# Kernel tuning notes

Hardware: AMD Instinct MI355X
Metric: run time of the kernel (lower is better)

## Reference

```python
import jax, jax.numpy as jnp
import numpy as np

FP8_MAX = 448.0  # float8_e4m3fn max
BLOCK = 128


def _quant_blocks_1d(x, bs=BLOCK, eps=1e-12):
    """Block-wise (along last dim) fp8 e4m3 quantization of activations.
    x: (M, K) float32 -> (x_q_f32 (M,K) on fp8 grid, scales (M, K//bs))."""
    M, K = x.shape
    xb = x.reshape(M, K // bs, bs)
    amax = jnp.max(jnp.abs(xb), axis=-1)                     # (M, Kb)
    s = jnp.maximum(amax / FP8_MAX, eps)                     # (M, Kb)
    xq = jnp.clip(xb / s[..., None], -FP8_MAX, FP8_MAX)
    xq = xq.astype(jnp.float8_e4m3fn).astype(jnp.float32)    # round to fp8 grid
    return xq.reshape(M, K), s


def _quant_weight_2d(w, bs=BLOCK, eps=1e-12):
    """2D block-wise fp8 quantization of weight (out, in) -> fp8-grid values + (Nb,Kb) scales."""
    N, K = w.shape
    wb = w.reshape(N // bs, bs, K // bs, bs)
    amax = jnp.max(jnp.abs(wb), axis=(1, 3))                 # (Nb, Kb)
    s = jnp.maximum(amax / FP8_MAX, eps)
    wq = jnp.clip(wb / s[:, None, :, None], -FP8_MAX, FP8_MAX)
    wq = wq.astype(jnp.float8_e4m3fn).astype(jnp.float32)
    return wq.reshape(N, K), s


def setup_inputs() -> dict:
    key = jax.random.key(0)
    kx, kw = jax.random.split(key)
    M, K, N = 4096, 2048, 8192
    x = jax.random.normal(kx, (M, K), dtype=jnp.float32)
    w = jax.random.normal(kw, (N, K), dtype=jnp.float32) * 0.02
    w_q, w_s = _quant_weight_2d(w)  # pre-quantized at "construction" time
    return {"x": x, "w_q": w_q, "w_s": w_s}


def reference(x, w_q, w_s):
    """FP8Linear forward (Triton path math): quantize x block-wise to fp8,
    block-scaled fp8 GEMM against fp8 weight with (Nb,Kb) weight scales.
    Math is identical to dequant-then-GEMM with fp32 accumulation."""
    bs = BLOCK
    M, K = x.shape
    N = w_q.shape[0]
    x_q, x_s = _quant_blocks_1d(x, bs)                        # (M,K), (M,K//bs)
    # dequantize (fold scales back in) — same values the fused kernel computes
    x_deq = (x_q.reshape(M, K // bs, bs) * x_s[..., None]).reshape(M, K)
    w_deq = (w_q.reshape(N // bs, bs, K // bs, bs) * w_s[:, None, :, None]).reshape(N, K)
    out = x_deq @ w_deq.T                                     # (M, N), fp32 accum
    return out
```

## Files before the change

### kernel.cpp

```cpp
#include <hip/hip_runtime.h>
#include <cstdint>
#include <cstddef>

static constexpr int M = 4096, K = 2048, N = 8192;
static constexpr int KBLK = K / 128;

#define GLOBAL_AS __attribute__((address_space(1)))
#define LDS_AS    __attribute__((address_space(3)))

typedef float f32x4 __attribute__((ext_vector_type(4)));
typedef int   i32x4 __attribute__((ext_vector_type(4)));
typedef int   i32x8 __attribute__((ext_vector_type(8)));


__device__ inline float fp8_e4m3_rne(float a) {
    float mag = fminf(fabsf(a), 448.0f);
    float r;
    if (mag < 0.015625f) {
        r = rintf(mag * 512.0f) * (1.0f / 512.0f);
    } else {
        uint32_t u = __float_as_uint(mag);
        u = (u + ((u >> 20) & 1u) + 0x7FFFFu) & 0xFFF00000u;
        r = fminf(__uint_as_float(u), 448.0f);
    }
    return copysignf(r, a);
}


__global__ void quant_x_kernel(const float* __restrict__ x, uint8_t* __restrict__ xq,
                               float* __restrict__ sxT) {
    int task = blockIdx.x * 8 + (threadIdx.x >> 5);
    int sub  = threadIdx.x & 31;
    int row = task >> 4;
    int kb  = task & 15;
    const float* p = x + (size_t)row * K + kb * 128 + sub * 4;
    float4 v = *reinterpret_cast<const float4*>(p);
    float amax = fmaxf(fmaxf(fabsf(v.x), fabsf(v.y)), fmaxf(fabsf(v.z), fabsf(v.w)));
    #pragma unroll
    for (int off = 16; off; off >>= 1) amax = fmaxf(amax, __shfl_xor(amax, off));
    float s = fmaxf(amax / 448.0f, 1e-12f);
    float q0 = fminf(fmaxf(v.x / s, -448.f), 448.f);
    float q1 = fminf(fmaxf(v.y / s, -448.f), 448.f);
    float q2 = fminf(fmaxf(v.z / s, -448.f), 448.f);
    float q3 = fminf(fmaxf(v.w / s, -448.f), 448.f);
    uint32_t pk = __builtin_amdgcn_cvt_pk_fp8_f32(q0, q1, 0, false);
    pk = __builtin_amdgcn_cvt_pk_fp8_f32(q2, q3, pk, true);
    *reinterpret_cast<uint32_t*>(xq + (size_t)row * K + kb * 128 + sub * 4) = pk;
    if (sub == 0) sxT[(size_t)kb * M + row] = s;
}

__global__ void quant_w_kernel(const float* __restrict__ wq, uint8_t* __restrict__ w8) {
    size_t i = ((size_t)blockIdx.x * blockDim.x + threadIdx.x) * 8;
    float4 a = *reinterpret_cast<const float4*>(wq + i);
    float4 b = *reinterpret_cast<const float4*>(wq + i + 4);
    uint32_t lo = __builtin_amdgcn_cvt_pk_fp8_f32(a.x, a.y, 0, false);
    lo = __builtin_amdgcn_cvt_pk_fp8_f32(a.z, a.w, lo, true);
    uint32_t hi = __builtin_amdgcn_cvt_pk_fp8_f32(b.x, b.y, 0, false);
    hi = __builtin_amdgcn_cvt_pk_fp8_f32(b.z, b.w, hi, true);
    uint2 o; o.x = lo; o.y = hi;
    *reinterpret_cast<uint2*>(w8 + i) = o;
}


__device__ __forceinline__ void stageA8(const uint8_t* __restrict__ g,
                                        uint8_t* l, int h, int tid) {
    #pragma unroll
    for (int i = 0; i < 2; ++i) {
        int t2 = tid + i * 512;
        int lr = t2 >> 3;
        int qs = t2 & 7;
        int r  = (lr >> 6) * 128 + h * 64 + (lr & 63);
        int s  = qs ^ (r & 7);
        int ks = ((s & 3) << 1) | (s >> 2);
        __builtin_amdgcn_global_load_lds(
            (const GLOBAL_AS uint32_t*)(g + (size_t)r * K + (ks << 4)),
            (LDS_AS uint32_t*)(l + r * 128 + qs * 16), 16, 0, 0);
    }
}

__device__ __forceinline__ void stageB8(const uint8_t* __restrict__ g,
                                        uint8_t* l, int h, int tid) {
    #pragma unroll
    for (int i = 0; i < 2; ++i) {
        int t2 = tid + i * 512;
        int lr = t2 >> 3;
        int qs = t2 & 7;
        int r  = (lr >> 5) * 64 + h * 32 + (lr & 31);
        int s  = qs ^ (r & 7);
        int ks = ((s & 3) << 1) | (s >> 2);
        __builtin_amdgcn_global_load_lds(
            (const GLOBAL_AS uint32_t*)(g + (size_t)r * K + (ks << 4)),
            (LDS_AS uint32_t*)(l + r * 128 + qs * 16), 16, 0, 0);
    }
}

#define LOAD_A(MH)                                                                \
  _Pragma("unroll")                                                               \
  for (int m = 0; m < 4; ++m) {                                                   \
    int row = wr * 128 + (MH) * 64 + m * 16 + (lane & 15);                        \
    const char* rp = (const char*)lAp + row * 128;                                \
    i32x4 lo = *(const i32x4*)(rp + (((lg)     ^ (row & 7)) << 4));               \
    i32x4 hi = *(const i32x4*)(rp + (((4 | lg) ^ (row & 7)) << 4));               \
    af[m] = __builtin_shufflevector(lo, hi, 0, 1, 2, 3, 4, 5, 6, 7);              \
    xs[m] = sxl[t * 256 + wr * 128 + (MH) * 64 + m * 16 + (lane & 15)];           \
  }

#define LOAD_B(NH)                                                                \
  _Pragma("unroll")                                                               \
  for (int n = 0; n < 2; ++n) {                                                   \
    int row = wc * 64 + (NH) * 32 + n * 16 + (lane & 15);                         \
    const char* rp = (const char*)lBp + row * 128;                                \
    i32x4 lo = *(const i32x4*)(rp + (((lg)     ^ (row & 7)) << 4));               \
    i32x4 hi = *(const i32x4*)(rp + (((4 | lg) ^ (row & 7)) << 4));               \
    bfr[n] = __builtin_shufflevector(lo, hi, 0, 1, 2, 3, 4, 5, 6, 7);             \
  }

#define QCOMP(MH, NH)                                                             \
  {                                                                               \
    f32x4 P[4][2];                                                                \
    __builtin_amdgcn_s_setprio(1);                                                \
    _Pragma("unroll")                                                             \
    for (int m = 0; m < 4; ++m)                                                   \
      _Pragma("unroll")                                                           \
      for (int n = 0; n < 2; ++n)                                                 \
        P[m][n] = __builtin_amdgcn_mfma_scale_f32_16x16x128_f8f6f4(               \
            bfr[n], af[m], zf4, 0, 0, 0, 0x7F7F7F7F, 0, 0x7F7F7F7F);              \
    __builtin_amdgcn_s_setprio(0);                                                \
    _Pragma("unroll")                                                             \
    for (int m = 0; m < 4; ++m) {                                                 \
      float sm = xs[m] * wst;                                                     \
      _Pragma("unroll")                                                           \
      for (int n = 0; n < 2; ++n)                                                 \
        acc[(MH) * 4 + m][(NH) * 2 + n] += sm * P[m][n];                          \
    }                                                                             \
  }

__global__ __launch_bounds__(512, 2) void gemm_kernel(
    const uint8_t* __restrict__ A, const uint8_t* __restrict__ B,
    const float* __restrict__ sxT_g, const float* __restrict__ Ws,
    float* __restrict__ C) {
    __shared__ uint8_t lA[2][256 * 128];
    __shared__ uint8_t lB[2][256 * 128];
    __shared__ float   sxl[KBLK * 256];
    __shared__ float   wsl[32];

    int cpx = gridDim.x >> 3;
    int sw  = (blockIdx.x & 7) * cpx + (blockIdx.x >> 3);
    int tm = sw & 15;
    int tn = sw >> 4;
    int row0 = tm * 256, col0 = tn * 256;

    int tid = threadIdx.x;
    int wid = tid >> 6, lane = tid & 63;
    int lg  = lane >> 4;
    int wr = wid >> 2, wc = wid & 3;

    const uint8_t* Ag = A + (size_t)row0 * K;
    const uint8_t* Bg = B + (size_t)col0 * K;

    f32x4 acc[8][4] = {};
    const f32x4 zf4 = {0.f, 0.f, 0.f, 0.f};

    if (tid < 32)
        __builtin_amdgcn_global_load_lds(
            (const GLOBAL_AS uint32_t*)(Ws + (tn * 2 + (tid >> 4)) * KBLK + (tid & 15)),
            (LDS_AS uint32_t*)(wsl + tid), 4, 0, 0);
    #pragma unroll
    for (int i = 0; i < 2; ++i) {
        int idx = tid + i * 512;
        __builtin_amdgcn_global_load_lds(
            (const GLOBAL_AS uint32_t*)(sxT_g + (size_t)(idx >> 6) * M + row0 + (idx & 63) * 4),
            (LDS_AS uint32_t*)(sxl + idx * 4), 16, 0, 0);
    }
    stageA8(Ag, lA[0], 0, tid);
    stageA8(Ag, lA[0], 1, tid);
    stageB8(Bg, lB[0], 0, tid);
    stageB8(Bg, lB[0], 1, tid);
    __syncthreads();

    for (int t = 0; t < KBLK; ++t) {
        const uint8_t* lAp = lA[t & 1];
        const uint8_t* lBp = lB[t & 1];
        uint8_t* sA = lA[(t + 1) & 1];
        uint8_t* sB = lB[(t + 1) & 1];
        int tn1 = (t + 1 < KBLK) ? (t + 1) : 0;
        const uint8_t* gA = Ag + (size_t)tn1 * 128;
        const uint8_t* gB = Bg + (size_t)tn1 * 128;
        bool stg = (t + 1 < KBLK);
        i32x8 af[4], bfr[2];
        float xs[4];
        float wst = wsl[(wc >> 1) * KBLK + t];

        LOAD_A(0); LOAD_B(0);
        if (stg) { stageA8(gA, sA, 0, tid); stageB8(gB, sB, 0, tid); }
        QCOMP(0, 0);
        LOAD_B(1);
        if (stg) stageB8(gB, sB, 1, tid);
        QCOMP(0, 1);
        LOAD_A(1);
        if (stg) stageA8(gA, sA, 1, tid);
        QCOMP(1, 1);
        LOAD_B(0);
        QCOMP(1, 0);

        __syncthreads();
    }

    #pragma unroll
    for (int m = 0; m < 8; ++m)
        #pragma unroll
        for (int j = 0; j < 4; ++j) {
            int rr = row0 + wr * 128 + m * 16 + (lane & 15);
            int cc = col0 + wc * 64 + j * 16 + (lane >> 4) * 4;
            *reinterpret_cast<f32x4*>(&C[(size_t)rr * N + cc]) = acc[m][j];
        }
}


__global__ void xs_kernel(const float* __restrict__ x, float* __restrict__ xs) {
    int task = blockIdx.x * 4 + (threadIdx.x >> 6);
    int lane = threadIdx.x & 63;
    int row = task >> 4, kb = task & 15;
    float2 v = *reinterpret_cast<const float2*>(x + (size_t)row * K + kb * 128 + lane * 2);
    float amax = fmaxf(fabsf(v.x), fabsf(v.y));
    #pragma unroll
    for (int off = 32; off; off >>= 1) amax = fmaxf(amax, __shfl_xor(amax, off));
    if (lane == 0) xs[row * KBLK + kb] = fmaxf(amax / 448.0f, 1e-12f);
}

__global__ __launch_bounds__(256) void fallback_gemm(const float* __restrict__ x,
                                                     const float* __restrict__ wq,
                                                     const float* __restrict__ wsc,
                                                     const float* __restrict__ xs,
                                                     float* __restrict__ C) {
    __shared__ float As[64][128];
    __shared__ float Bs[64][128];
    int tm = blockIdx.x % (M / 64), tn = blockIdx.x / (M / 64);
    int row0 = tm * 64, col0 = tn * 64;
    int tid = threadIdx.x;
    int tr = tid >> 4, tc = tid & 15;
    float acc[4][4] = {};
    for (int kb = 0; kb < KBLK; ++kb) {
        int k0 = kb * 128;
        __syncthreads();
        for (int t = tid * 4; t < 64 * 128; t += 256 * 4) {
            int r = t >> 7, c = t & 127;
            float4 va = *reinterpret_cast<const float4*>(x + (size_t)(row0 + r) * K + k0 + c);
            float sa = xs[(row0 + r) * KBLK + kb];
            va.x = fp8_e4m3_rne(va.x / sa) * sa; va.y = fp8_e4m3_rne(va.y / sa) * sa;
            va.z = fp8_e4m3_rne(va.z / sa) * sa; va.w = fp8_e4m3_rne(va.w / sa) * sa;
            *reinterpret_cast<float4*>(&As[r][c]) = va;
            float4 vb = *reinterpret_cast<const float4*>(wq + (size_t)(col0 + r) * K + k0 + c);
            float sb = wsc[((col0 + r) >> 7) * KBLK + kb];
            vb.x *= sb; vb.y *= sb; vb.z *= sb; vb.w *= sb;
            *reinterpret_cast<float4*>(&Bs[r][c]) = vb;
        }
        __syncthreads();
        for (int kk = 0; kk < 128; ++kk) {
            float a[4], b[4];
            #pragma unroll
            for (int i = 0; i < 4; ++i) a[i] = As[tr * 4 + i][kk];
            #pragma unroll
            for (int j = 0; j < 4; ++j) b[j] = Bs[tc * 4 + j][kk];
            #pragma unroll
            for (int i = 0; i < 4; ++i)
                #pragma unroll
                for (int j = 0; j < 4; ++j) acc[i][j] += a[i] * b[j];
        }
    }
    #pragma unroll
    for (int i = 0; i < 4; ++i)
        #pragma unroll
        for (int j = 0; j < 4; ++j)
            C[(size_t)(row0 + tr * 4 + i) * N + col0 + tc * 4 + j] = acc[i][j];
}


extern "C" void kernel_launch(void* const* d_in, const int* in_sizes, int n_in,
                              void* d_out, int out_size, void* d_ws, size_t ws_size,
                              hipStream_t stream) {
    const float* x  = (const float*)d_in[0];
    const float* wq = (const float*)d_in[1];
    const float* ws = (const float*)d_in[2];
    float* out = (float*)d_out;

    size_t need_fast = (size_t)M * K + (size_t)N * K + (size_t)KBLK * M * 4;
    if (ws_size >= need_fast) {
        uint8_t* xq8 = (uint8_t*)d_ws;
        uint8_t* w8  = xq8 + (size_t)M * K;
        float*   sxT = (float*)(w8 + (size_t)N * K);
        quant_x_kernel<<<M * KBLK / 8, 256, 0, stream>>>(x, xq8, sxT);
        quant_w_kernel<<<(int)(((size_t)N * K / 8) / 256), 256, 0, stream>>>(wq, w8);
        gemm_kernel<<<(M / 256) * (N / 256), 512, 0, stream>>>(xq8, w8, sxT, ws, out);
    } else if (ws_size >= (size_t)M * KBLK * 4) {
        float* xs = (float*)d_ws;
        xs_kernel<<<M * KBLK / 4, 256, 0, stream>>>(x, xs);
        fallback_gemm<<<(M / 64) * (N / 64), 256, 0, stream>>>(x, wq, ws, xs, out);
    }
}
```

Measured before the change: 115.4 us.

## Software-pipeline MFMA batches with rescale and fragment loads in GEMM loop

Restructures the per-K-block inner loop so that each batch of scaled MFMAs is issued before the previous batch's per-block rescale FMAs and the next fragment LDS loads. This lets VALU rescale work and LDS reads overlap with matrix-core execution. All four global-to-LDS staging calls for the next tile are now issued together up front, and the s_setprio hints are removed. In exchange the kernel holds more live registers (double B fragments, two scale arrays, two partial-product sets), which raises register pressure under the 512x2 launch bound.

```diff
diff --git a/kernel.cpp b/kernel.cpp
--- a/kernel.cpp
+++ b/kernel.cpp
@@ -94,45 +94,42 @@
     }
 }
 
-#define LOAD_A(MH)                                                                \
+#define LOAD_AF(MH, AFV, XSV)                                                     \
   _Pragma("unroll")                                                               \
   for (int m = 0; m < 4; ++m) {                                                   \
     int row = wr * 128 + (MH) * 64 + m * 16 + (lane & 15);                        \
     const char* rp = (const char*)lAp + row * 128;                                \
     i32x4 lo = *(const i32x4*)(rp + (((lg)     ^ (row & 7)) << 4));               \
     i32x4 hi = *(const i32x4*)(rp + (((4 | lg) ^ (row & 7)) << 4));               \
-    af[m] = __builtin_shufflevector(lo, hi, 0, 1, 2, 3, 4, 5, 6, 7);              \
-    xs[m] = sxl[t * 256 + wr * 128 + (MH) * 64 + m * 16 + (lane & 15)];           \
+    AFV[m] = __builtin_shufflevector(lo, hi, 0, 1, 2, 3, 4, 5, 6, 7);             \
+    XSV[m] = sxl[t * 256 + wr * 128 + (MH) * 64 + m * 16 + (lane & 15)];          \
   }
 
-#define LOAD_B(NH)                                                                \
+#define LOAD_BF(NH, BFV)                                                          \
   _Pragma("unroll")                                                               \
   for (int n = 0; n < 2; ++n) {                                                   \
     int row = wc * 64 + (NH) * 32 + n * 16 + (lane & 15);                         \
     const char* rp = (const char*)lBp + row * 128;                                \
     i32x4 lo = *(const i32x4*)(rp + (((lg)     ^ (row & 7)) << 4));               \
     i32x4 hi = *(const i32x4*)(rp + (((4 | lg) ^ (row & 7)) << 4));               \
-    bfr[n] = __builtin_shufflevector(lo, hi, 0, 1, 2, 3, 4, 5, 6, 7);             \
+    BFV[n] = __builtin_shufflevector(lo, hi, 0, 1, 2, 3, 4, 5, 6, 7);             \
   }
 
-#define QCOMP(MH, NH)                                                             \
-  {                                                                               \
-    f32x4 P[4][2];                                                                \
-    __builtin_amdgcn_s_setprio(1);                                                \
+#define MFMA8(PD, AFV, BFV)                                                       \
+  _Pragma("unroll")                                                               \
+  for (int m = 0; m < 4; ++m)                                                     \
     _Pragma("unroll")                                                             \
-    for (int m = 0; m < 4; ++m)                                                   \
-      _Pragma("unroll")                                                           \
-      for (int n = 0; n < 2; ++n)                                                 \
-        P[m][n] = __builtin_amdgcn_mfma_scale_f32_16x16x128_f8f6f4(               \
-            bfr[n], af[m], zf4, 0, 0, 0, 0x7F7F7F7F, 0, 0x7F7F7F7F);              \
-    __builtin_amdgcn_s_setprio(0);                                                \
+    for (int n = 0; n < 2; ++n)                                                   \
+      PD[m][n] = __builtin_amdgcn_mfma_scale_f32_16x16x128_f8f6f4(                \
+          BFV[n], AFV[m], zf4, 0, 0, 0, 0x7F7F7F7F, 0, 0x7F7F7F7F);
+
+#define RESC(PD, XSV, MH, NH)                                                     \
+  _Pragma("unroll")                                                               \
+  for (int m = 0; m < 4; ++m) {                                                   \
+    float sm = XSV[m] * wst;                                                      \
     _Pragma("unroll")                                                             \
-    for (int m = 0; m < 4; ++m) {                                                 \
-      float sm = xs[m] * wst;                                                     \
-      _Pragma("unroll")                                                           \
-      for (int n = 0; n < 2; ++n)                                                 \
-        acc[(MH) * 4 + m][(NH) * 2 + n] += sm * P[m][n];                          \
-    }                                                                             \
+    for (int n = 0; n < 2; ++n)                                                   \
+      acc[(MH) * 4 + m][(NH) * 2 + n] += sm * PD[m][n];                           \
   }
 
 __global__ __launch_bounds__(512, 2) void gemm_kernel(
@@ -187,21 +184,29 @@
         const uint8_t* gA = Ag + (size_t)tn1 * 128;
         const uint8_t* gB = Bg + (size_t)tn1 * 128;
         bool stg = (t + 1 < KBLK);
-        i32x8 af[4], bfr[2];
-        float xs[4];
+        i32x8 af[4], bfe[2], bfo[2];
+        float xs0[4], xs1[4];
         float wst = wsl[(wc >> 1) * KBLK + t];
 
-        LOAD_A(0); LOAD_B(0);
-        if (stg) { stageA8(gA, sA, 0, tid); stageB8(gB, sB, 0, tid); }
-        QCOMP(0, 0);
-        LOAD_B(1);
-        if (stg) stageB8(gB, sB, 1, tid);
-        QCOMP(0, 1);
-        LOAD_A(1);
-        if (stg) stageA8(gA, sA, 1, tid);
-        QCOMP(1, 1);
-        LOAD_B(0);
-        QCOMP(1, 0);
+        LOAD_AF(0, af, xs0);
+        LOAD_BF(0, bfe);
+        if (stg) {
+            stageA8(gA, sA, 0, tid);
+            stageA8(gA, sA, 1, tid);
+            stageB8(gB, sB, 0, tid);
+            stageB8(gB, sB, 1, tid);
+        }
+        f32x4 P0[4][2]; MFMA8(P0, af, bfe);
+        LOAD_BF(1, bfo);
+        RESC(P0, xs0, 0, 0);
+        f32x4 P1[4][2]; MFMA8(P1, af, bfo);
+        LOAD_AF(1, af, xs1);
+        RESC(P1, xs0, 0, 1);
+        f32x4 P2[4][2]; MFMA8(P2, af, bfo);
+        LOAD_BF(0, bfe);
+        RESC(P2, xs1, 1, 1);
+        f32x4 P3[4][2]; MFMA8(P3, af, bfe);
+        RESC(P3, xs1, 1, 0);
 
         __syncthreads();
     }
```

Measured after the change: 116.8 us. Within noise of the previous version (+1.2%).
